# Kernel tuning notes

Hardware: AMD Instinct MI355X
Metric: run time of the kernel (lower is better)

Reference implementation:

```python
import jax, jax.numpy as jnp
import numpy as np
from math import sqrt, log

B, P, C = 8, 256, 512          # batch, patch_size, input_channel
R, M = 64, 256                 # rule_num, model_size
VARPI_1, VARPI_2, TAU_0 = 0.01, 0.001, 0.9
EPS = float(np.finfo(np.float32).tiny)


def setup_inputs() -> dict:
    key = jax.random.key(0)
    ks = jax.random.split(key, 6)

    def xavier(k, shape):
        fan_out, fan_in = shape
        bound = sqrt(6.0 / (fan_in + fan_out))
        return jax.random.uniform(k, shape, jnp.float32, -bound, bound)

    sigma0 = sqrt(-M / (2.0 * (R + 1) * (R + 1) * log(0.5)))
    return {
        "input_data": jax.random.normal(ks[0], (B, P, C), jnp.float32),
        "Wq": xavier(ks[1], (M, P)),      "bq": jnp.zeros((M,), jnp.float32),
        "Wk": xavier(ks[2], (M * R, P)),  "bk": jnp.zeros((M * R,), jnp.float32),
        "Wv": xavier(ks[3], (M * R, P)),  "bv": jnp.zeros((M * R,), jnp.float32),
        "Wo": xavier(ks[4], (P, M)),      "bo": jnp.zeros((P,), jnp.float32),
        "sigma": jnp.full((R, M), sigma0, jnp.float32),
    }


def reference(input_data, Wq, bq, Wk, bk, Wv, bv, Wo, bo, sigma):
    tau = TAU_0 * (1.0 / (R + EPS)) ** (1.0 / M)
    x = jnp.transpose(input_data, (0, 2, 1))            # [B,C,P]
    q = x @ Wq.T + bq                                   # [B,C,M]
    k = (x @ Wk.T + bk).reshape(B, C, R, M)
    v = (x @ Wv.T + bv).reshape(B, C, R, M)

    dist = (q[:, :, None, :] - k) / (sigma + EPS)       # [B,C,R,M]
    fire = jnp.exp(-0.5 / M * jnp.sum(dist * dist, axis=-1)) + EPS   # [B,C,R]
    nfs = fire / (jnp.sum(fire, axis=-1, keepdims=True) + EPS)

    # nucleus-style top-p mask over rule dim (no grad)
    s = jax.lax.stop_gradient(nfs)
    sorted_desc = -jnp.sort(-s, axis=-1)
    err = jnp.cumsum(sorted_desc, axis=-1) - tau
    err = jnp.where(err < 0, jnp.ones_like(err), err)
    idx = jnp.argmin(err, axis=-1)                      # [B,C]
    thresh = jnp.take_along_axis(sorted_desc, idx[..., None], axis=-1)  # [B,C,1]
    mask = (s >= thresh).astype(jnp.float32)

    nfs = nfs * mask
    nfs = nfs / (jnp.sum(nfs, axis=-1, keepdims=True) + EPS)

    pred = jnp.einsum('bcr,bcrm->bcm', nfs, v)          # dropout is identity in eval
    out = jnp.transpose(pred @ Wo.T + bo, (0, 2, 1))    # [B,P,C]

    # constraint loss
    eye = jnp.eye(M, dtype=jnp.float32)
    weight_loss = jnp.linalg.norm(Wq @ Wo - eye)
    bias_loss = jnp.linalg.norm(bq) + jnp.linalg.norm(bo)
    key_l1 = jnp.sum(jnp.abs(Wk)) + jnp.sum(jnp.abs(bk))
    val_l1 = jnp.sum(jnp.abs(Wv)) + jnp.sum(jnp.abs(bv))
    loss = VARPI_1 * (weight_loss + bias_loss) + VARPI_2 * (key_l1 + val_l1)
    return out, loss
```

## Files before the change

### kernel.cpp

```cpp
#include <hip/hip_runtime.h>
#include <math.h>

#define EPS_F 1.1754943508222875e-38f

typedef __attribute__((ext_vector_type(8))) _Float16 half8;
typedef __attribute__((ext_vector_type(4))) float f32x4;
typedef __attribute__((ext_vector_type(8))) unsigned short ushort8;

__device__ __forceinline__ unsigned short f2h(float f) {
  _Float16 h = (_Float16)f;
  return __builtin_bit_cast(unsigned short, h);
}
__device__ __forceinline__ float h2f(unsigned short u) {
  return (float)__builtin_bit_cast(_Float16, u);
}

__device__ __forceinline__ void gload16(const void* g, void* l) {
  __builtin_amdgcn_global_load_lds(
      (const __attribute__((address_space(1))) void*)g,
      (__attribute__((address_space(3))) void*)l, 16, 0, 0);
}

__global__ __launch_bounds__(256) void k_prep_x(const float* __restrict__ in,
                                                unsigned short* __restrict__ x) {
  __shared__ float t[32][33];
  int c0 = blockIdx.x * 32, p0 = blockIdx.y * 32, b = blockIdx.z;
  int tx = threadIdx.x & 31, ty = threadIdx.x >> 5;
#pragma unroll
  for (int i = ty; i < 32; i += 8)
    t[i][tx] = in[(b * 256 + p0 + i) * 512 + c0 + tx];
  __syncthreads();
#pragma unroll
  for (int i = ty; i < 32; i += 8)
    x[(b * 512 + c0 + i) * 256 + p0 + tx] = f2h(t[tx][i]);
}

__global__ __launch_bounds__(256) void k_prep_w(
    const float* __restrict__ Wq, const float* __restrict__ Wk,
    const float* __restrict__ Wv, const float* __restrict__ Wo,
    const float* __restrict__ bq, const float* __restrict__ bk,
    const float* __restrict__ sigma,
    unsigned short* __restrict__ wd, unsigned short* __restrict__ woh,
    unsigned short* __restrict__ wqh, float* __restrict__ bdr,
    float* __restrict__ pbk, float* __restrict__ pbv) {
  __shared__ float r1[4], r2[4];
  int gid = blockIdx.x * 256 + threadIdx.x;
  int i4 = gid * 4;
  int rm = i4 >> 8, p = i4 & 255, m = rm & 255;
  const float4 wk = *(const float4*)(Wk + i4);
  const float4 wv = *(const float4*)(Wv + i4);
  const float4 wq = *(const float4*)(Wq + m * 256 + p);
  float rs = 1.0f / (sigma[rm] + EPS_F);
  ushort4 d;
  d.x = f2h((wq.x - wk.x) * rs); d.y = f2h((wq.y - wk.y) * rs);
  d.z = f2h((wq.z - wk.z) * rs); d.w = f2h((wq.w - wk.w) * rs);
  *(ushort4*)(wd + i4) = d;
  float ak = fabsf(wk.x) + fabsf(wk.y) + fabsf(wk.z) + fabsf(wk.w);
  float av = fabsf(wv.x) + fabsf(wv.y) + fabsf(wv.z) + fabsf(wv.w);
  if (p == 0) bdr[rm] = (bq[m] - bk[rm]) * rs;
  if (gid < 65536) {
    woh[gid] = f2h(Wo[gid]);
    ushort4 q4;
    q4.x = f2h(wq.x); q4.y = f2h(wq.y); q4.z = f2h(wq.z); q4.w = f2h(wq.w);
    *(ushort4*)(wqh + i4) = q4;
  }
  int lane = threadIdx.x & 63, w = threadIdx.x >> 6;
#pragma unroll
  for (int dlt = 1; dlt < 64; dlt <<= 1) {
    ak += __shfl_xor(ak, dlt);
    av += __shfl_xor(av, dlt);
  }
  if (lane == 0) { r1[w] = ak; r2[w] = av; }
  __syncthreads();
  if (threadIdx.x == 0) {
    pbk[blockIdx.x] = r1[0] + r1[1] + r1[2] + r1[3];
    pbv[blockIdx.x] = r2[0] + r2[1] + r2[2] + r2[3];
  }
}

__global__ __launch_bounds__(256) void k_tv(const float* __restrict__ Wv,
                                            const float* __restrict__ Wo,
                                            unsigned short* __restrict__ wvT,
                                            unsigned short* __restrict__ woT) {
  __shared__ float t[32][33];
  int r = blockIdx.z;
  int tx = threadIdx.x & 31, ty = threadIdx.x >> 5;
  if (r < 64) {
    int p0 = blockIdx.x * 32, m0 = blockIdx.y * 32;
#pragma unroll
    for (int i = ty; i < 32; i += 8)
      t[i][tx] = Wv[(size_t)(r * 256 + m0 + i) * 256 + p0 + tx];
    __syncthreads();
#pragma unroll
    for (int i = ty; i < 32; i += 8)
      wvT[(size_t)r * 65536 + (p0 + i) * 256 + m0 + tx] = f2h(t[tx][i]);
  } else {
    int p0 = blockIdx.x * 32, m0 = blockIdx.y * 32;
#pragma unroll
    for (int i = ty; i < 32; i += 8)
      t[i][tx] = Wo[(p0 + i) * 256 + m0 + tx];
    __syncthreads();
#pragma unroll
    for (int i = ty; i < 32; i += 8)
      woT[(m0 + i) * 256 + p0 + tx] = f2h(t[tx][i]);
  }
}

__global__ __launch_bounds__(256) void k_wqwo(const unsigned short* __restrict__ wqh,
                                              const unsigned short* __restrict__ woT,
                                              float* __restrict__ pbw) {
  __shared__ unsigned short As[128 * 64];
  __shared__ unsigned short Bs[128 * 64];
  __shared__ float red4[4];
  const int tid = threadIdx.x, w = tid >> 6, lane = tid & 63;
  const int wr = w >> 1, wc = w & 1, cl = lane & 15, kg = lane >> 4;
  const int bx = blockIdx.x, by = blockIdx.y;

  f32x4 acc[4][4];
#pragma unroll
  for (int i = 0; i < 4; ++i)
#pragma unroll
    for (int j = 0; j < 4; ++j) acc[i][j] = (f32x4){0.f, 0.f, 0.f, 0.f};

  for (int t = 0; t < 4; ++t) {
    const int kc = t * 64;
    __syncthreads();
#pragma unroll
    for (int j = 0; j < 4; ++j) {
      int s = w * 4 + j;
      int ch = s * 64 + lane;
      int row = ch >> 3, c = ch & 7;
      gload16(wqh + (by * 128 + row) * 256 + kc + ((c ^ (row & 7)) << 3),
              As + s * 512);
      gload16(woT + (bx * 128 + row) * 256 + kc + ((c ^ (row & 7)) << 3),
              Bs + s * 512);
    }
    __syncthreads();
#pragma unroll
    for (int kk = 0; kk < 2; ++kk) {
      half8 a[4], b[4];
      int g = kk * 4 + kg;
#pragma unroll
      for (int i = 0; i < 4; ++i) {
        int row = wr * 64 + i * 16 + cl;
        a[i] = *(const half8*)(As + row * 64 + ((g ^ (row & 7)) << 3));
      }
#pragma unroll
      for (int j = 0; j < 4; ++j) {
        int n = wc * 64 + j * 16 + cl;
        b[j] = *(const half8*)(Bs + n * 64 + ((g ^ (n & 7)) << 3));
      }
#pragma unroll
      for (int i = 0; i < 4; ++i)
#pragma unroll
        for (int j = 0; j < 4; ++j)
          acc[i][j] = __builtin_amdgcn_mfma_f32_16x16x32_f16(a[i], b[j], acc[i][j], 0, 0, 0);
    }
  }
  float s = 0.f;
#pragma unroll
  for (int i = 0; i < 4; ++i)
#pragma unroll
    for (int q = 0; q < 4; ++q) {
      int rg = by * 128 + wr * 64 + i * 16 + kg * 4 + q;
#pragma unroll
      for (int j = 0; j < 4; ++j) {
        int cg = bx * 128 + wc * 64 + j * 16 + cl;
        float dd = acc[i][j][q] - (rg == cg ? 1.0f : 0.0f);
        s += dd * dd;
      }
    }
#pragma unroll
  for (int d = 1; d < 64; d <<= 1) s += __shfl_xor(s, d);
  if (lane == 0) red4[w] = s;
  __syncthreads();
  if (tid == 0) pbw[by * 2 + bx] = red4[0] + red4[1] + red4[2] + red4[3];
}

__global__ __launch_bounds__(256) void k_gw(const unsigned short* __restrict__ woh,
                                            const unsigned short* __restrict__ wvT,
                                            unsigned short* __restrict__ G) {
  __shared__ unsigned short As[128 * 64];
  __shared__ unsigned short Bs[128 * 64];
  const int tid = threadIdx.x, w = tid >> 6, lane = tid & 63;
  const int wr = w >> 1, wc = w & 1, cl = lane & 15, kg = lane >> 4;
  const int pl = blockIdx.x, ph = blockIdx.y, r = blockIdx.z;

  f32x4 acc[4][4];
#pragma unroll
  for (int i = 0; i < 4; ++i)
#pragma unroll
    for (int j = 0; j < 4; ++j) acc[i][j] = (f32x4){0.f, 0.f, 0.f, 0.f};

  for (int t = 0; t < 4; ++t) {
    const int kc = t * 64;
    __syncthreads();
#pragma unroll
    for (int j = 0; j < 4; ++j) {
      int s = w * 4 + j;
      int ch = s * 64 + lane;
      int row = ch >> 3, c = ch & 7;
      gload16(woh + (ph * 128 + row) * 256 + kc + ((c ^ (row & 7)) << 3),
              As + s * 512);
      gload16(wvT + (size_t)r * 65536 + (pl * 128 + row) * 256 + kc +
                  ((c ^ (row & 7)) << 3),
              Bs + s * 512);
    }
    __syncthreads();
#pragma unroll
    for (int kk = 0; kk < 2; ++kk) {
      half8 a[4], b[4];
      int g = kk * 4 + kg;
#pragma unroll
      for (int i = 0; i < 4; ++i) {
        int row = wr * 64 + i * 16 + cl;
        a[i] = *(const half8*)(As + row * 64 + ((g ^ (row & 7)) << 3));
      }
#pragma unroll
      for (int j = 0; j < 4; ++j) {
        int n = wc * 64 + j * 16 + cl;
        b[j] = *(const half8*)(Bs + n * 64 + ((g ^ (n & 7)) << 3));
      }
#pragma unroll
      for (int i = 0; i < 4; ++i)
#pragma unroll
        for (int j = 0; j < 4; ++j)
          acc[i][j] = __builtin_amdgcn_mfma_f32_16x16x32_f16(a[i], b[j], acc[i][j], 0, 0, 0);
    }
  }
#pragma unroll
  for (int i = 0; i < 4; ++i)
#pragma unroll
    for (int q = 0; q < 4; ++q) {
      int pr = ph * 128 + wr * 64 + i * 16 + kg * 4 + q;
#pragma unroll
      for (int j = 0; j < 4; ++j) {
        int pc = pl * 128 + wc * 64 + j * 16 + cl;
        G[(size_t)r * 65536 + pr * 256 + pc] = f2h(acc[i][j][q]);
      }
    }
}

__global__ __launch_bounds__(256) void k_hv(const unsigned short* __restrict__ woh,
                                            const float* __restrict__ bv,
                                            float* __restrict__ hv) {
  __shared__ float bvl[256];
  int r = blockIdx.x, t = threadIdx.x;
  bvl[t] = bv[r * 256 + t];
  __syncthreads();
  float s = 0.f;
#pragma unroll 8
  for (int c8 = 0; c8 < 32; ++c8) {
    ushort8 wv8 = *(const ushort8*)(woh + t * 256 + c8 * 8);
#pragma unroll
    for (int e = 0; e < 8; ++e) s = fmaf(h2f(wv8[e]), bvl[c8 * 8 + e], s);
  }
  hv[r * 256 + t] = s;
}

__global__ __launch_bounds__(256, 2) void k_fire(
    const unsigned short* __restrict__ xh, const unsigned short* __restrict__ wd,
    const float* __restrict__ bdr, float* __restrict__ fire_p) {
  __shared__ unsigned short As[128 * 64];
  __shared__ unsigned short Bs[256 * 64];
  __shared__ float red[128][2];
  const int tid = threadIdx.x, w = tid >> 6, lane = tid & 63;
  const int wr = w >> 1, wc = w & 1, cl = lane & 15, kg = lane >> 4;
  const int wg = blockIdx.x;
  const int swz = (wg & 7) * 256 + (wg >> 3);
  const int bc0 = (swz & 31) * 128, r = swz >> 5;

  float bdrv[8];
#pragma unroll
  for (int j = 0; j < 8; ++j)
    bdrv[j] = bdr[r * 256 + wc * 128 + j * 16 + cl];

  f32x4 acc[4][8];
#pragma unroll
  for (int i = 0; i < 4; ++i)
#pragma unroll
    for (int j = 0; j < 8; ++j) acc[i][j] = (f32x4){0.f, 0.f, 0.f, 0.f};

  for (int t = 0; t < 4; ++t) {
    const int kc = t * 64;
    __syncthreads();
#pragma unroll
    for (int j = 0; j < 4; ++j) {
      int s = w * 4 + j;
      int ch = s * 64 + lane;
      int row = ch >> 3, c = ch & 7;
      gload16(xh + (size_t)(bc0 + row) * 256 + kc + ((c ^ (row & 7)) << 3),
              As + s * 512);
    }
#pragma unroll
    for (int j = 0; j < 8; ++j) {
      int s = w * 8 + j;
      int ch = s * 64 + lane;
      int n = ch >> 3, c = ch & 7;
      gload16(wd + (size_t)r * 65536 + n * 256 + kc + ((c ^ (n & 7)) << 3),
              Bs + s * 512);
    }
    __syncthreads();
#pragma unroll
    for (int kk = 0; kk < 2; ++kk) {
      half8 a[4], b[8];
      int g = kk * 4 + kg;
#pragma unroll
      for (int i = 0; i < 4; ++i) {
        int row = wr * 64 + i * 16 + cl;
        a[i] = *(const half8*)(As + row * 64 + ((g ^ (row & 7)) << 3));
      }
#pragma unroll
      for (int j = 0; j < 8; ++j) {
        int n = wc * 128 + j * 16 + cl;
        b[j] = *(const half8*)(Bs + n * 64 + ((g ^ (n & 7)) << 3));
      }
#pragma unroll
      for (int i = 0; i < 4; ++i)
#pragma unroll
        for (int j = 0; j < 8; ++j)
          acc[i][j] = __builtin_amdgcn_mfma_f32_16x16x32_f16(a[i], b[j], acc[i][j], 0, 0, 0);
    }
  }
  float rowsum[4][4];
#pragma unroll
  for (int i = 0; i < 4; ++i)
#pragma unroll
    for (int q = 0; q < 4; ++q) {
      float s2 = 0.f;
#pragma unroll
      for (int j = 0; j < 8; ++j) {
        float t2 = acc[i][j][q] + bdrv[j];
        s2 += t2 * t2;
      }
      rowsum[i][q] = s2;
    }
#pragma unroll
  for (int dlt = 1; dlt < 16; dlt <<= 1)
#pragma unroll
    for (int i = 0; i < 4; ++i)
#pragma unroll
      for (int q = 0; q < 4; ++q) rowsum[i][q] += __shfl_xor(rowsum[i][q], dlt);
  if (cl == 0) {
#pragma unroll
    for (int i = 0; i < 4; ++i)
#pragma unroll
      for (int q = 0; q < 4; ++q)
        red[wr * 64 + i * 16 + kg * 4 + q][wc] = rowsum[i][q];
  }
  __syncthreads();
  if (tid < 128)
    fire_p[(size_t)(bc0 + tid) * 64 + r] = red[tid][0] + red[tid][1];
}

__global__ __launch_bounds__(256) void k_mask(const float* __restrict__ fire_p,
                                              float* __restrict__ nfs, float tau) {
  int w = threadIdx.x >> 6, lane = threadIdx.x & 63;
  int bc = blockIdx.x * 4 + w;
  size_t ix = (size_t)bc * 64 + lane;
  float f = expf(-0.001953125f * fire_p[ix]) + EPS_F;
  float tot = f;
#pragma unroll
  for (int d = 1; d < 64; d <<= 1) tot += __shfl_xor(tot, d);
  float nf = f / (tot + EPS_F);
  float v = nf;
#pragma unroll
  for (int k = 2; k <= 64; k <<= 1) {
#pragma unroll
    for (int j = 32; j > 0; j >>= 1) {
      if (j >= k) continue;
      float o = __shfl_xor(v, j);
      bool lower = (lane & j) == 0;
      bool desc = (lane & k) == 0;
      float mn = fminf(v, o), mx = fmaxf(v, o);
      v = (desc == lower) ? mx : mn;
    }
  }
  float cs = v;
#pragma unroll
  for (int d = 1; d < 64; d <<= 1) {
    float t = __shfl_up(cs, d);
    if (lane >= d) cs += t;
  }
  float err = cs - tau;
  if (err < 0.f) err = 1.0f;
  float mn = err;
#pragma unroll
  for (int d = 1; d < 64; d <<= 1) mn = fminf(mn, __shfl_xor(mn, d));
  unsigned long long ball = __ballot(err == mn);
  int idx = __ffsll(ball) - 1;
  float thresh = __shfl(v, idx);
  float keep = (nf >= thresh) ? nf : 0.0f;
  float tot2 = keep;
#pragma unroll
  for (int d = 1; d < 64; d <<= 1) tot2 += __shfl_xor(tot2, d);
  nfs[ix] = keep / (tot2 + EPS_F);
}

__global__ __launch_bounds__(512, 4) void k_predg(
    const unsigned short* __restrict__ xh, const unsigned short* __restrict__ G,
    const float* __restrict__ nfs, const float* __restrict__ hv,
    unsigned short* __restrict__ pp) {
  __shared__ unsigned short As[128 * 64];
  __shared__ unsigned short Bs[128 * 64];
  __shared__ float nl[128][9];
  const int tid = threadIdx.x, w = tid >> 6, lane = tid & 63;
  const int wr = w >> 1, wc = w & 1, cl = lane & 15, kg = lane >> 4;
  const int wg = blockIdx.x;
  const int swz = (wg & 7) * 64 + (wg >> 3);
  const int sl = swz >> 6, inner = swz & 63;
  const int bc0 = ((inner >> 1) & 31) * 128, ph = inner & 1;

  for (int e = tid; e < 1024; e += 512)
    nl[e >> 3][e & 7] = nfs[(size_t)(bc0 + (e >> 3)) * 64 + sl * 8 + (e & 7)];

  f32x4 acc[2][4];
#pragma unroll
  for (int i = 0; i < 2; ++i)
#pragma unroll
    for (int j = 0; j < 4; ++j) acc[i][j] = (f32x4){0.f, 0.f, 0.f, 0.f};

  _Float16 nlh[2];
  for (int t = 0; t < 32; ++t) {
    const int rr = t >> 2, kc = (t & 3) * 64;
    __syncthreads();
#pragma unroll
    for (int j = 0; j < 2; ++j) {
      int s = w * 2 + j;
      int ch = s * 64 + lane;
      int row = ch >> 3, c = ch & 7;
      gload16(xh + (size_t)(bc0 + row) * 256 + kc + ((c ^ (row & 7)) << 3),
              As + s * 512);
      gload16(G + (size_t)(sl * 8 + rr) * 65536 + (ph * 128 + row) * 256 + kc +
                  ((c ^ (row & 7)) << 3),
              Bs + s * 512);
    }
    __syncthreads();
    if ((t & 3) == 0) {
#pragma unroll
      for (int i = 0; i < 2; ++i)
        nlh[i] = (_Float16)nl[wr * 32 + i * 16 + cl][rr];
    }
#pragma unroll
    for (int kk = 0; kk < 2; ++kk) {
      half8 a[2], b[4];
      int g = kk * 4 + kg;
#pragma unroll
      for (int i = 0; i < 2; ++i) {
        int row = wr * 32 + i * 16 + cl;
        a[i] = *(const half8*)(As + row * 64 + ((g ^ (row & 7)) << 3));
        a[i] = a[i] * nlh[i];
      }
#pragma unroll
      for (int j = 0; j < 4; ++j) {
        int n = wc * 64 + j * 16 + cl;
        b[j] = *(const half8*)(Bs + n * 64 + ((g ^ (n & 7)) << 3));
      }
#pragma unroll
      for (int i = 0; i < 2; ++i)
#pragma unroll
        for (int j = 0; j < 4; ++j)
          acc[i][j] = __builtin_amdgcn_mfma_f32_16x16x32_f16(a[i], b[j], acc[i][j], 0, 0, 0);
    }
  }
  float hvv[8][4];
#pragma unroll
  for (int j = 0; j < 4; ++j) {
    int col = ph * 128 + wc * 64 + j * 16 + cl;
#pragma unroll
    for (int rr = 0; rr < 8; ++rr)
      hvv[rr][j] = hv[(sl * 8 + rr) * 256 + col];
  }
  unsigned short* base = pp + (size_t)sl * 1048576;
#pragma unroll
  for (int i = 0; i < 2; ++i)
#pragma unroll
    for (int q = 0; q < 4; ++q) {
      int outrow = wr * 32 + i * 16 + kg * 4 + q;
      float nlv[8];
#pragma unroll
      for (int rr = 0; rr < 8; ++rr) nlv[rr] = nl[outrow][rr];
#pragma unroll
      for (int j = 0; j < 4; ++j) {
        float s = acc[i][j][q];
#pragma unroll
        for (int rr = 0; rr < 8; ++rr) s = fmaf(nlv[rr], hvv[rr][j], s);
        int col = ph * 128 + wc * 64 + j * 16 + cl;
        base[(size_t)(bc0 + outrow) * 256 + col] = f2h(s);
      }
    }
}

__global__ __launch_bounds__(256) void k_finalout(const unsigned short* __restrict__ pp,
                                                  const float* __restrict__ bo,
                                                  float* __restrict__ out) {
  __shared__ float sacc[256][33];
  __shared__ float bol[256];
  const int tid = threadIdx.x;
  bol[tid] = bo[tid];
  const int bc0 = blockIdx.x * 32;
  const int b = bc0 >> 9, c0 = bc0 & 511;
#pragma unroll
  for (int i = 0; i < 4; ++i) {
    int unit = tid + 256 * i;
    int pch = unit & 31, lbc = unit >> 5;
    float s[8];
#pragma unroll
    for (int e = 0; e < 8; ++e) s[e] = 0.f;
#pragma unroll
    for (int sl = 0; sl < 8; ++sl) {
      ushort8 v = *(const ushort8*)(pp + (size_t)sl * 1048576 +
                                    (size_t)(bc0 + lbc) * 256 + pch * 8);
#pragma unroll
      for (int e = 0; e < 8; ++e) s[e] += h2f(v[e]);
    }
#pragma unroll
    for (int e = 0; e < 8; ++e) sacc[pch * 8 + e][lbc] = s[e];
  }
  __syncthreads();
  const int p = tid;
  float bov = bol[p];
  float* dst = out + (size_t)b * 131072 + (size_t)p * 512 + c0;
#pragma unroll
  for (int e0 = 0; e0 < 8; ++e0) {
    float4 v;
    v.x = sacc[p][e0 * 4 + 0] + bov;
    v.y = sacc[p][e0 * 4 + 1] + bov;
    v.z = sacc[p][e0 * 4 + 2] + bov;
    v.w = sacc[p][e0 * 4 + 3] + bov;
    *(float4*)(dst + e0 * 4) = v;
  }
}

__global__ __launch_bounds__(1024) void k_final(
    const float* __restrict__ bq, const float* __restrict__ bk,
    const float* __restrict__ bv, const float* __restrict__ bo,
    const float* __restrict__ pbw, const float* __restrict__ pbk,
    const float* __restrict__ pbv, float* __restrict__ loss_out) {
  __shared__ float r[16][5];
  const int tid = threadIdx.x;
  float swq = (tid < 4) ? pbw[tid] : 0.f;
  float sbk = 0.f, sbv = 0.f;
  for (int i = tid; i < 4096; i += 1024) {
    sbk += pbk[i];
    sbv += pbv[i];
  }
  for (int i = tid; i < 16384; i += 1024) {
    sbk += fabsf(bk[i]);
    sbv += fabsf(bv[i]);
  }
  float sbq = 0.f, sbo = 0.f;
  if (tid < 256) {
    float a = bq[tid];
    sbq = a * a;
    float b = bo[tid];
    sbo = b * b;
  }
  int lane = tid & 63, w = tid >> 6;
#pragma unroll
  for (int d = 1; d < 64; d <<= 1) {
    swq += __shfl_xor(swq, d);
    sbk += __shfl_xor(sbk, d);
    sbv += __shfl_xor(sbv, d);
    sbq += __shfl_xor(sbq, d);
    sbo += __shfl_xor(sbo, d);
  }
  if (lane == 0) {
    r[w][0] = swq; r[w][1] = sbk; r[w][2] = sbv; r[w][3] = sbq; r[w][4] = sbo;
  }
  __syncthreads();
  if (tid == 0) {
    float t[5] = {0.f, 0.f, 0.f, 0.f, 0.f};
    for (int i = 0; i < 16; ++i)
      for (int j = 0; j < 5; ++j) t[j] += r[i][j];
    float loss = 0.01f * (sqrtf(t[0]) + sqrtf(t[3]) + sqrtf(t[4])) +
                 0.001f * (t[1] + t[2]);
    *loss_out = loss;
  }
}

extern "C" void kernel_launch(void* const* d_in, const int* in_sizes, int n_in,
                              void* d_out, int out_size, void* d_ws, size_t ws_size,
                              hipStream_t stream) {
  const float* in    = (const float*)d_in[0];
  const float* Wq    = (const float*)d_in[1];
  const float* bq    = (const float*)d_in[2];
  const float* Wk    = (const float*)d_in[3];
  const float* bk    = (const float*)d_in[4];
  const float* Wv    = (const float*)d_in[5];
  const float* bv    = (const float*)d_in[6];
  const float* Wo    = (const float*)d_in[7];
  const float* bo    = (const float*)d_in[8];
  const float* sigma = (const float*)d_in[9];
  float* out = (float*)d_out;

  char* ws = (char*)d_ws;
  unsigned short* xh     = (unsigned short*)(ws);
  unsigned short* woh    = (unsigned short*)(ws + 2097152);
  float*          bdr    = (float*)(ws + 2228224);
  float*          nfs    = (float*)(ws + 2293760);
  float*          fire_p = (float*)(ws + 3342336);
  float*          pbk    = (float*)(ws + 4390912);
  float*          pbv    = (float*)(ws + 4407296);
  float*          pbw    = (float*)(ws + 4423680);
  float*          hv     = (float*)(ws + 4424704);
  unsigned short* wd     = (unsigned short*)(ws + 4718592);
  unsigned short* wvT    = (unsigned short*)(ws + 13107200);
  unsigned short* pp     = (unsigned short*)(ws + 4718592);
  unsigned short* G      = (unsigned short*)(ws + 21495808);
  unsigned short* wqh    = (unsigned short*)(ws + 29884416);
  unsigned short* woT    = (unsigned short*)(ws + 30015488);

  k_prep_x<<<dim3(16, 8, 8), 256, 0, stream>>>(in, xh);
  k_prep_w<<<4096, 256, 0, stream>>>(Wq, Wk, Wv, Wo, bq, bk, sigma,
                                     wd, woh, wqh, bdr, pbk, pbv);
  k_tv<<<dim3(8, 8, 65), 256, 0, stream>>>(Wv, Wo, wvT, woT);
  k_wqwo<<<dim3(2, 2), 256, 0, stream>>>(wqh, woT, pbw);
  k_gw<<<dim3(2, 2, 64), 256, 0, stream>>>(woh, wvT, G);
  k_hv<<<64, 256, 0, stream>>>(woh, bv, hv);
  k_fire<<<2048, 256, 0, stream>>>(xh, wd, bdr, fire_p);
  const float tau = (float)(0.9 * pow(1.0 / (64.0 + (double)EPS_F), 1.0 / 256.0));
  k_mask<<<1024, 256, 0, stream>>>(fire_p, nfs, tau);
  k_predg<<<512, 512, 0, stream>>>(xh, G, nfs, hv, pp);
  k_finalout<<<128, 256, 0, stream>>>(pp, bo, out);
  k_final<<<1, 1024, 0, stream>>>(bq, bk, bv, bo, pbw, pbk, pbv, out + 1048576);
}
```

Baseline: 143.3 us.

## Merge weight-prep kernels and weight GEMMs into fewer launches

```diff
diff --git a/kernel.cpp b/kernel.cpp
--- a/kernel.cpp
+++ b/kernel.cpp
@@ -35,227 +35,194 @@
     x[(b * 512 + c0 + i) * 256 + p0 + tx] = f2h(t[tx][i]);
 }
 
-__global__ __launch_bounds__(256) void k_prep_w(
+__global__ __launch_bounds__(256) void k_prepwt(
     const float* __restrict__ Wq, const float* __restrict__ Wk,
     const float* __restrict__ Wv, const float* __restrict__ Wo,
     const float* __restrict__ bq, const float* __restrict__ bk,
     const float* __restrict__ sigma,
     unsigned short* __restrict__ wd, unsigned short* __restrict__ woh,
     unsigned short* __restrict__ wqh, float* __restrict__ bdr,
-    float* __restrict__ pbk, float* __restrict__ pbv) {
-  __shared__ float r1[4], r2[4];
-  int gid = blockIdx.x * 256 + threadIdx.x;
-  int i4 = gid * 4;
-  int rm = i4 >> 8, p = i4 & 255, m = rm & 255;
-  const float4 wk = *(const float4*)(Wk + i4);
-  const float4 wv = *(const float4*)(Wv + i4);
-  const float4 wq = *(const float4*)(Wq + m * 256 + p);
-  float rs = 1.0f / (sigma[rm] + EPS_F);
-  ushort4 d;
-  d.x = f2h((wq.x - wk.x) * rs); d.y = f2h((wq.y - wk.y) * rs);
-  d.z = f2h((wq.z - wk.z) * rs); d.w = f2h((wq.w - wk.w) * rs);
-  *(ushort4*)(wd + i4) = d;
-  float ak = fabsf(wk.x) + fabsf(wk.y) + fabsf(wk.z) + fabsf(wk.w);
-  float av = fabsf(wv.x) + fabsf(wv.y) + fabsf(wv.z) + fabsf(wv.w);
-  if (p == 0) bdr[rm] = (bq[m] - bk[rm]) * rs;
-  if (gid < 65536) {
-    woh[gid] = f2h(Wo[gid]);
-    ushort4 q4;
-    q4.x = f2h(wq.x); q4.y = f2h(wq.y); q4.z = f2h(wq.z); q4.w = f2h(wq.w);
-    *(ushort4*)(wqh + i4) = q4;
-  }
-  int lane = threadIdx.x & 63, w = threadIdx.x >> 6;
-#pragma unroll
-  for (int dlt = 1; dlt < 64; dlt <<= 1) {
-    ak += __shfl_xor(ak, dlt);
-    av += __shfl_xor(av, dlt);
-  }
-  if (lane == 0) { r1[w] = ak; r2[w] = av; }
-  __syncthreads();
-  if (threadIdx.x == 0) {
-    pbk[blockIdx.x] = r1[0] + r1[1] + r1[2] + r1[3];
-    pbv[blockIdx.x] = r2[0] + r2[1] + r2[2] + r2[3];
-  }
-}
-
-__global__ __launch_bounds__(256) void k_tv(const float* __restrict__ Wv,
-                                            const float* __restrict__ Wo,
-                                            unsigned short* __restrict__ wvT,
-                                            unsigned short* __restrict__ woT) {
+    float* __restrict__ pbk, unsigned short* __restrict__ wvT,
+    unsigned short* __restrict__ woT, float* __restrict__ pbv) {
   __shared__ float t[32][33];
-  int r = blockIdx.z;
-  int tx = threadIdx.x & 31, ty = threadIdx.x >> 5;
-  if (r < 64) {
-    int p0 = blockIdx.x * 32, m0 = blockIdx.y * 32;
-#pragma unroll
-    for (int i = ty; i < 32; i += 8)
-      t[i][tx] = Wv[(size_t)(r * 256 + m0 + i) * 256 + p0 + tx];
+  __shared__ float r1[4];
+  const int bid = blockIdx.x;
+  const int lane = threadIdx.x & 63, w = threadIdx.x >> 6;
+  if (bid < 4096) {
+    int gid = bid * 256 + threadIdx.x;
+    int i4 = gid * 4;
+    int rm = i4 >> 8, p = i4 & 255, m = rm & 255;
+    const float4 wk = *(const float4*)(Wk + i4);
+    const float4 wq = *(const float4*)(Wq + m * 256 + p);
+    float rs = 1.0f / (sigma[rm] + EPS_F);
+    ushort4 d;
+    d.x = f2h((wq.x - wk.x) * rs); d.y = f2h((wq.y - wk.y) * rs);
+    d.z = f2h((wq.z - wk.z) * rs); d.w = f2h((wq.w - wk.w) * rs);
+    *(ushort4*)(wd + i4) = d;
+    float ak = fabsf(wk.x) + fabsf(wk.y) + fabsf(wk.z) + fabsf(wk.w);
+    if (p == 0) bdr[rm] = (bq[m] - bk[rm]) * rs;
+    if (gid < 65536) {
+      woh[gid] = f2h(Wo[gid]);
+      ushort4 q4;
+      q4.x = f2h(wq.x); q4.y = f2h(wq.y); q4.z = f2h(wq.z); q4.w = f2h(wq.w);
+      *(ushort4*)(wqh + i4) = q4;
+    }
+#pragma unroll
+    for (int dlt = 1; dlt < 64; dlt <<= 1) ak += __shfl_xor(ak, dlt);
+    if (lane == 0) r1[w] = ak;
     __syncthreads();
-#pragma unroll
-    for (int i = ty; i < 32; i += 8)
-      wvT[(size_t)r * 65536 + (p0 + i) * 256 + m0 + tx] = f2h(t[tx][i]);
+    if (threadIdx.x == 0)
+      pbk[bid] = r1[0] + r1[1] + r1[2] + r1[3];
   } else {
-    int p0 = blockIdx.x * 32, m0 = blockIdx.y * 32;
-#pragma unroll
-    for (int i = ty; i < 32; i += 8)
-      t[i][tx] = Wo[(p0 + i) * 256 + m0 + tx];
-    __syncthreads();
-#pragma unroll
-    for (int i = ty; i < 32; i += 8)
-      woT[(m0 + i) * 256 + p0 + tx] = f2h(t[tx][i]);
-  }
-}
-
-__global__ __launch_bounds__(256) void k_wqwo(const unsigned short* __restrict__ wqh,
-                                              const unsigned short* __restrict__ woT,
-                                              float* __restrict__ pbw) {
+    int tt = bid - 4096;
+    int z = tt >> 6, rem = tt & 63;
+    int bx = rem & 7, by = rem >> 3;
+    int tx = threadIdx.x & 31, ty = threadIdx.x >> 5;
+    if (z < 64) {
+      int p0 = bx * 32, m0 = by * 32, r = z;
+      float av = 0.f;
+#pragma unroll
+      for (int i = ty; i < 32; i += 8) {
+        float v = Wv[(size_t)(r * 256 + m0 + i) * 256 + p0 + tx];
+        t[i][tx] = v;
+        av += fabsf(v);
+      }
+      __syncthreads();
+#pragma unroll
+      for (int i = ty; i < 32; i += 8)
+        wvT[(size_t)r * 65536 + (p0 + i) * 256 + m0 + tx] = f2h(t[tx][i]);
+#pragma unroll
+      for (int d = 1; d < 64; d <<= 1) av += __shfl_xor(av, d);
+      if (lane == 0) r1[w] = av;
+      __syncthreads();
+      if (threadIdx.x == 0)
+        pbv[r * 64 + by * 8 + bx] = r1[0] + r1[1] + r1[2] + r1[3];
+    } else {
+      int p0 = bx * 32, m0 = by * 32;
+#pragma unroll
+      for (int i = ty; i < 32; i += 8)
+        t[i][tx] = Wo[(p0 + i) * 256 + m0 + tx];
+      __syncthreads();
+#pragma unroll
+      for (int i = ty; i < 32; i += 8)
+        woT[(m0 + i) * 256 + p0 + tx] = f2h(t[tx][i]);
+    }
+  }
+}
+
+__global__ __launch_bounds__(256) void k_gwx(
+    const unsigned short* __restrict__ woh, const unsigned short* __restrict__ wvT,
+    const unsigned short* __restrict__ wqh, const unsigned short* __restrict__ woT,
+    const float* __restrict__ bv,
+    unsigned short* __restrict__ G, float* __restrict__ pbw,
+    float* __restrict__ hv) {
   __shared__ unsigned short As[128 * 64];
   __shared__ unsigned short Bs[128 * 64];
   __shared__ float red4[4];
+  __shared__ float bvl[256];
+  const int bid = blockIdx.x;
   const int tid = threadIdx.x, w = tid >> 6, lane = tid & 63;
   const int wr = w >> 1, wc = w & 1, cl = lane & 15, kg = lane >> 4;
-  const int bx = blockIdx.x, by = blockIdx.y;
-
-  f32x4 acc[4][4];
-#pragma unroll
-  for (int i = 0; i < 4; ++i)
-#pragma unroll
-    for (int j = 0; j < 4; ++j) acc[i][j] = (f32x4){0.f, 0.f, 0.f, 0.f};
-
-  for (int t = 0; t < 4; ++t) {
-    const int kc = t * 64;
-    __syncthreads();
-#pragma unroll
-    for (int j = 0; j < 4; ++j) {
-      int s = w * 4 + j;
-      int ch = s * 64 + lane;
-      int row = ch >> 3, c = ch & 7;
-      gload16(wqh + (by * 128 + row) * 256 + kc + ((c ^ (row & 7)) << 3),
-              As + s * 512);
-      gload16(woT + (bx * 128 + row) * 256 + kc + ((c ^ (row & 7)) << 3),
-              Bs + s * 512);
-    }
-    __syncthreads();
-#pragma unroll
-    for (int kk = 0; kk < 2; ++kk) {
-      half8 a[4], b[4];
-      int g = kk * 4 + kg;
-#pragma unroll
-      for (int i = 0; i < 4; ++i) {
-        int row = wr * 64 + i * 16 + cl;
-        a[i] = *(const half8*)(As + row * 64 + ((g ^ (row & 7)) << 3));
-      }
+
+  if (bid < 260) {
+    const bool isgw = bid < 256;
+    const int r = bid >> 2;
+    const int rowbase = isgw ? (((bid >> 1) & 1) * 128) : (((bid - 256) >> 1) * 128);
+    const int colbase = isgw ? ((bid & 1) * 128) : (((bid - 256) & 1) * 128);
+    const unsigned short* Aglob = isgw ? woh : wqh;
+    const unsigned short* Bglob = isgw ? (wvT + (size_t)r * 65536) : woT;
+
+    f32x4 acc[4][4];
+#pragma unroll
+    for (int i = 0; i < 4; ++i)
+#pragma unroll
+      for (int j = 0; j < 4; ++j) acc[i][j] = (f32x4){0.f, 0.f, 0.f, 0.f};
+
+    for (int tks = 0; tks < 4; ++tks) {
+      const int kc = tks * 64;
+      __syncthreads();
 #pragma unroll
       for (int j = 0; j < 4; ++j) {
-        int n = wc * 64 + j * 16 + cl;
-        b[j] = *(const half8*)(Bs + n * 64 + ((g ^ (n & 7)) << 3));
-      }
+        int s = w * 4 + j;
+        int ch = s * 64 + lane;
+        int row = ch >> 3, c = ch & 7;
+        gload16(Aglob + (rowbase + row) * 256 + kc + ((c ^ (row & 7)) << 3),
+                As + s * 512);
+        gload16(Bglob + (colbase + row) * 256 + kc + ((c ^ (row & 7)) << 3),
+                Bs + s * 512);
+      }
+      __syncthreads();
+#pragma unroll
+      for (int kk = 0; kk < 2; ++kk) {
+        half8 a[4], b[4];
+        int g = kk * 4 + kg;
+#pragma unroll
+        for (int i = 0; i < 4; ++i) {
+          int row = wr * 64 + i * 16 + cl;
+          a[i] = *(const half8*)(As + row * 64 + ((g ^ (row & 7)) << 3));
+        }
+#pragma unroll
+        for (int j = 0; j < 4; ++j) {
+          int n = wc * 64 + j * 16 + cl;
+          b[j] = *(const half8*)(Bs + n * 64 + ((g ^ (n & 7)) << 3));
+        }
+#pragma unroll
+        for (int i = 0; i < 4; ++i)
+#pragma unroll
+          for (int j = 0; j < 4; ++j)
+            acc[i][j] = __builtin_amdgcn_mfma_f32_16x16x32_f16(a[i], b[j], acc[i][j], 0, 0, 0);
+      }
+    }
+    if (isgw) {
 #pragma unroll
       for (int i = 0; i < 4; ++i)
 #pragma unroll
-        for (int j = 0; j < 4; ++j)
-          acc[i][j] = __builtin_amdgcn_mfma_f32_16x16x32_f16(a[i], b[j], acc[i][j], 0, 0, 0);
-    }
-  }
-  float s = 0.f;
-#pragma unroll
-  for (int i = 0; i < 4; ++i)
-#pragma unroll
-    for (int q = 0; q < 4; ++q) {
-      int rg = by * 128 + wr * 64 + i * 16 + kg * 4 + q;
-#pragma unroll
-      for (int j = 0; j < 4; ++j) {
-        int cg = bx * 128 + wc * 64 + j * 16 + cl;
-        float dd = acc[i][j][q] - (rg == cg ? 1.0f : 0.0f);
-        s += dd * dd;
-      }
-    }
-#pragma unroll
-  for (int d = 1; d < 64; d <<= 1) s += __shfl_xor(s, d);
-  if (lane == 0) red4[w] = s;
-  __syncthreads();
-  if (tid == 0) pbw[by * 2 + bx] = red4[0] + red4[1] + red4[2] + red4[3];
-}
-
-__global__ __launch_bounds__(256) void k_gw(const unsigned short* __restrict__ woh,
-                                            const unsigned short* __restrict__ wvT,
-                                            unsigned short* __restrict__ G) {
-  __shared__ unsigned short As[128 * 64];
-  __shared__ unsigned short Bs[128 * 64];
-  const int tid = threadIdx.x, w = tid >> 6, lane = tid & 63;
-  const int wr = w >> 1, wc = w & 1, cl = lane & 15, kg = lane >> 4;
-  const int pl = blockIdx.x, ph = blockIdx.y, r = blockIdx.z;
-
-  f32x4 acc[4][4];
-#pragma unroll
-  for (int i = 0; i < 4; ++i)
-#pragma unroll
-    for (int j = 0; j < 4; ++j) acc[i][j] = (f32x4){0.f, 0.f, 0.f, 0.f};
-
-  for (int t = 0; t < 4; ++t) {
-    const int kc = t * 64;
-    __syncthreads();
-#pragma unroll
-    for (int j = 0; j < 4; ++j) {
-      int s = w * 4 + j;
-      int ch = s * 64 + lane;
-      int row = ch >> 3, c = ch & 7;
-      gload16(woh + (ph * 128 + row) * 256 + kc + ((c ^ (row & 7)) << 3),
-              As + s * 512);
-      gload16(wvT + (size_t)r * 65536 + (pl * 128 + row) * 256 + kc +
-                  ((c ^ (row & 7)) << 3),
-              Bs + s * 512);
-    }
-    __syncthreads();
-#pragma unroll
-    for (int kk = 0; kk < 2; ++kk) {
-      half8 a[4], b[4];
-      int g = kk * 4 + kg;
-#pragma unroll
-      for (int i = 0; i < 4; ++i) {
-        int row = wr * 64 + i * 16 + cl;
-        a[i] = *(const half8*)(As + row * 64 + ((g ^ (row & 7)) << 3));
-      }
-#pragma unroll
-      for (int j = 0; j < 4; ++j) {
-        int n = wc * 64 + j * 16 + cl;
-        b[j] = *(const half8*)(Bs + n * 64 + ((g ^ (n & 7)) << 3));
-      }
+        for (int q = 0; q < 4; ++q) {
+          int pr = rowbase + wr * 64 + i * 16 + kg * 4 + q;
+#pragma unroll
+          for (int j = 0; j < 4; ++j) {
+            int pc = colbase + wc * 64 + j * 16 + cl;
+            G[(size_t)r * 65536 + pr * 256 + pc] = f2h(acc[i][j][q]);
+          }
+        }
+    } else {
+      float s = 0.f;
 #pragma unroll
       for (int i = 0; i < 4; ++i)
 #pragma unroll
-        for (int j = 0; j < 4; ++j)
-          acc[i][j] = __builtin_amdgcn_mfma_f32_16x16x32_f16(a[i], b[j], acc[i][j], 0, 0, 0);
-    }
-  }
-#pragma unroll
-  for (int i = 0; i < 4; ++i)
-#pragma unroll
-    for (int q = 0; q < 4; ++q) {
-      int pr = ph * 128 + wr * 64 + i * 16 + kg * 4 + q;
-#pragma unroll
-      for (int j = 0; j < 4; ++j) {
-        int pc = pl * 128 + wc * 64 + j * 16 + cl;
-        G[(size_t)r * 65536 + pr * 256 + pc] = f2h(acc[i][j][q]);
-      }
-    }
-}
-
-__global__ __launch_bounds__(256) void k_hv(const unsigned short* __restrict__ woh,
-                                            const float* __restrict__ bv,
-                                            float* __restrict__ hv) {
-  __shared__ float bvl[256];
-  int r = blockIdx.x, t = threadIdx.x;
-  bvl[t] = bv[r * 256 + t];
-  __syncthreads();
-  float s = 0.f;
+        for (int q = 0; q < 4; ++q) {
+          int rg = rowbase + wr * 64 + i * 16 + kg * 4 + q;
+#pragma unroll
+          for (int j = 0; j < 4; ++j) {
+            int cg = colbase + wc * 64 + j * 16 + cl;
+            float dd = acc[i][j][q] - (rg == cg ? 1.0f : 0.0f);
+            s += dd * dd;
+          }
+        }
+#pragma unroll
+      for (int d = 1; d < 64; d <<= 1) s += __shfl_xor(s, d);
+      if (lane == 0) red4[w] = s;
+      __syncthreads();
+      if (tid == 0)
+        pbw[bid - 256] = red4[0] + red4[1] + red4[2] + red4[3];
+    }
+  } else {
+    int rb = (bid - 260) * 16;
+    for (int rr = 0; rr < 16; ++rr) {
+      int r = rb + rr;
+      bvl[tid] = bv[r * 256 + tid];
+      __syncthreads();
+      float s = 0.f;
 #pragma unroll 8
-  for (int c8 = 0; c8 < 32; ++c8) {
-    ushort8 wv8 = *(const ushort8*)(woh + t * 256 + c8 * 8);
-#pragma unroll
-    for (int e = 0; e < 8; ++e) s = fmaf(h2f(wv8[e]), bvl[c8 * 8 + e], s);
-  }
-  hv[r * 256 + t] = s;
+      for (int c8 = 0; c8 < 32; ++c8) {
+        ushort8 wv8 = *(const ushort8*)(woh + tid * 256 + c8 * 8);
+#pragma unroll
+        for (int e = 0; e < 8; ++e) s = fmaf(h2f(wv8[e]), bvl[c8 * 8 + e], s);
+      }
+      hv[r * 256 + tid] = s;
+      __syncthreads();
+    }
+  }
 }
 
 __global__ __launch_bounds__(256, 2) void k_fire(
@@ -612,12 +579,9 @@
   unsigned short* woT    = (unsigned short*)(ws + 30015488);
 
   k_prep_x<<<dim3(16, 8, 8), 256, 0, stream>>>(in, xh);
-  k_prep_w<<<4096, 256, 0, stream>>>(Wq, Wk, Wv, Wo, bq, bk, sigma,
-                                     wd, woh, wqh, bdr, pbk, pbv);
-  k_tv<<<dim3(8, 8, 65), 256, 0, stream>>>(Wv, Wo, wvT, woT);
-  k_wqwo<<<dim3(2, 2), 256, 0, stream>>>(wqh, woT, pbw);
-  k_gw<<<dim3(2, 2, 64), 256, 0, stream>>>(woh, wvT, G);
-  k_hv<<<64, 256, 0, stream>>>(woh, bv, hv);
+  k_prepwt<<<8256, 256, 0, stream>>>(Wq, Wk, Wv, Wo, bq, bk, sigma,
+                                     wd, woh, wqh, bdr, pbk, wvT, woT, pbv);
+  k_gwx<<<264, 256, 0, stream>>>(woh, wvT, wqh, woT, bv, G, pbw, hv);
   k_fire<<<2048, 256, 0, stream>>>(xh, wd, bdr, fire_p);
   const float tau = (float)(0.9 * pow(1.0 / (64.0 + (double)EPS_F), 1.0 / 256.0));
   k_mask<<<1024, 256, 0, stream>>>(fire_p, nfs, tau);
```

Result: slower. 186.3 us (+30.0%).
